# Kernel optimization log

Measured on AMD Instinct MI355X. Metric: run time of the kernel, lower is better.

The kernel has to match this reference:

```python
import jax, jax.numpy as jnp
import numpy as np
from jax import lax

N = 400000
INC = 128
MIDC = 64
OUTC = 128
KVOL = 27
EPS = 1e-5


def _bn(h, g, b, m, v):
    return (h - m) * (g * lax.rsqrt(v + EPS)) + b


def setup_inputs() -> dict:
    key = jax.random.key(0)
    ks = jax.random.split(key, 16)
    x = jax.random.normal(ks[0], (N, INC), jnp.float32)
    nb = jax.random.randint(ks[1], (KVOL, N), 0, N, jnp.int32)
    s1 = 1.0 / np.sqrt(INC)
    s2 = 1.0 / np.sqrt(MIDC * KVOL)
    s3 = 1.0 / np.sqrt(MIDC)
    w1 = jax.random.normal(ks[2], (INC, MIDC), jnp.float32) * s1
    w2 = jax.random.normal(ks[3], (KVOL, MIDC, MIDC), jnp.float32) * s2
    w3 = jax.random.normal(ks[4], (MIDC, OUTC), jnp.float32) * s3
    def bn_params(k, c):
        k1, k2, k3, k4 = jax.random.split(k, 4)
        return (jax.random.normal(k1, (c,), jnp.float32) * 0.1 + 1.0,
                jax.random.normal(k2, (c,), jnp.float32) * 0.1,
                jax.random.normal(k3, (c,), jnp.float32) * 0.1,
                jax.random.uniform(k4, (c,), jnp.float32) + 0.5)
    bn1_g, bn1_b, bn1_m, bn1_v = bn_params(ks[5], MIDC)
    bn2_g, bn2_b, bn2_m, bn2_v = bn_params(ks[6], MIDC)
    bn3_g, bn3_b, bn3_m, bn3_v = bn_params(ks[7], OUTC)
    return dict(x=x, nb=nb, w1=w1, w2=w2, w3=w3,
                bn1_g=bn1_g, bn1_b=bn1_b, bn1_m=bn1_m, bn1_v=bn1_v,
                bn2_g=bn2_g, bn2_b=bn2_b, bn2_m=bn2_m, bn2_v=bn2_v,
                bn3_g=bn3_g, bn3_b=bn3_b, bn3_m=bn3_m, bn3_v=bn3_v)


def reference(x, nb, w1, w2, w3,
              bn1_g, bn1_b, bn1_m, bn1_v,
              bn2_g, bn2_b, bn2_m, bn2_v,
              bn3_g, bn3_b, bn3_m, bn3_v):
    # 1x1 sparse conv == pointwise matmul
    h = jax.nn.relu(_bn(x @ w1, bn1_g, bn1_b, bn1_m, bn1_v))  # [N, midc]

    # ks=3 sparse conv: gather-matmul-accumulate over 27 kernel offsets
    def body(acc, kw):
        idx, wk = kw  # idx: [N] gather indices, wk: [midc, midc]
        return acc + h[idx] @ wk, None
    acc0 = jnp.zeros((N, MIDC), h.dtype)
    h2, _ = lax.scan(body, acc0, (nb, w2))
    h2 = jax.nn.relu(_bn(h2, bn2_g, bn2_b, bn2_m, bn2_v))

    # 1x1 conv + BN, then residual add (identity downsample: inc==outc, stride==1)
    h3 = _bn(h2 @ w3, bn3_g, bn3_b, bn3_m, bn3_v)  # [N, outc]
    return jax.nn.relu(h3 + x)
```

## Files before the change

kernel.cpp:

```cpp
#include <hip/hip_runtime.h>

#define N_PTS 400000
#define EPS 1e-5f
#define H_DELTA (11.0f / 255.0f)
#define H_INV_DELTA (255.0f / 11.0f)

typedef __attribute__((ext_vector_type(8))) short short8;
typedef __attribute__((ext_vector_type(4))) float f32x4;
typedef __attribute__((ext_vector_type(2))) float f32x2;
typedef __attribute__((ext_vector_type(2))) unsigned long long ull2;

constexpr size_t H_OFF   = 0;
constexpr size_t H2_OFF  = 51200000;
constexpr size_t W1T_OFF = 102400000;
constexpr size_t W2S_OFF = W1T_OFF + 16384;
constexpr size_t W3T_OFF = W2S_OFF + 221184;
constexpr size_t BNC_OFF = W3T_OFF + 16384;

__device__ __forceinline__ short f2bf(float f) {
  unsigned u = __builtin_bit_cast(unsigned, f);
  u += 0x7FFFu + ((u >> 16) & 1u);
  return (short)(u >> 16);
}

__device__ __forceinline__ unsigned cvtpk(float a, float b) {
  unsigned r;
  asm("v_cvt_pk_bf16_f32 %0, %1, %2" : "=v"(r) : "v"(a), "v"(b));
  return r;
}

__device__ __forceinline__ short8 q2bf(unsigned long long v) {
  unsigned lo = (unsigned)v, hi = (unsigned)(v >> 32);
  union { unsigned u[4]; short8 s8; } r;
  r.u[0] = cvtpk((float)(lo & 0xff), (float)((lo >> 8) & 0xff));
  r.u[1] = cvtpk((float)((lo >> 16) & 0xff), (float)(lo >> 24));
  r.u[2] = cvtpk((float)(hi & 0xff), (float)((hi >> 8) & 0xff));
  r.u[3] = cvtpk((float)((hi >> 16) & 0xff), (float)(hi >> 24));
  return r.s8;
}

__global__ __launch_bounds__(256) void prep_kernel(
    const float* __restrict__ w1, const float* __restrict__ w2,
    const float* __restrict__ w3,
    const float* __restrict__ g1, const float* __restrict__ b1,
    const float* __restrict__ m1, const float* __restrict__ v1,
    const float* __restrict__ g2, const float* __restrict__ b2,
    const float* __restrict__ m2, const float* __restrict__ v2,
    const float* __restrict__ g3, const float* __restrict__ b3,
    const float* __restrict__ m3, const float* __restrict__ v3,
    short* __restrict__ w1t, short* __restrict__ w2s,
    short* __restrict__ w3t, float* __restrict__ bnc) {
  int tid = blockIdx.x * 256 + threadIdx.x;
  int gs = gridDim.x * 256;
  for (int i = tid; i < 128 * 64; i += gs) {
    int k = i >> 6, n = i & 63;
    w1t[n * 128 + k] = f2bf(w1[i]);
  }
  for (int i = tid; i < 27 * 64 * 64; i += gs) {
    int kk = i >> 12, r = i & 4095, k = r >> 6, n = r & 63;
    int byte = (n * 64 + k) * 2;
    byte ^= (n & 7) << 4;
    w2s[kk * 4096 + (byte >> 1)] = f2bf(w2[i]);
  }
  for (int i = tid; i < 64 * 128; i += gs) {
    int k = i >> 7, n = i & 127;
    w3t[n * 64 + k] = f2bf(w3[i]);
  }
  if (tid < 64) {
    float s = g1[tid] * rsqrtf(v1[tid] + EPS);
    bnc[tid] = s; bnc[64 + tid] = b1[tid] - m1[tid] * s;
  } else if (tid < 128) {
    int c = tid - 64;
    float s = g2[c] * rsqrtf(v2[c] + EPS);
    bnc[128 + c] = s; bnc[192 + c] = b2[c] - m2[c] * s;
  } else if (tid < 256) {
    int c = tid - 128;
    float s = g3[c] * rsqrtf(v3[c] + EPS);
    bnc[256 + c] = s; bnc[384 + c] = b3[c] - m3[c] * s;
  }
}

__global__ __launch_bounds__(256) void stage1_kernel(
    const float* __restrict__ x, const short* __restrict__ w1t,
    const float* __restrict__ bnc, unsigned char* __restrict__ h) {
  __shared__ __align__(16) unsigned char t1[4][16][80];
  const int lane = threadIdx.x & 63;
  const int wid = threadIdx.x >> 6;
  const int lr = lane & 15, lk = lane >> 4;
  const long wbase = ((long)blockIdx.x * 4 + wid) * 64;
  if (wbase >= N_PTS) return;

  short8 bf[4][4];
#pragma unroll
  for (int nf = 0; nf < 4; ++nf)
#pragma unroll
    for (int ks = 0; ks < 4; ++ks)
      bf[nf][ks] = *(const short8*)(w1t + (nf * 16 + lr) * 128 + ks * 32 + lk * 8);

  float s[4], t[4];
#pragma unroll
  for (int nf = 0; nf < 4; ++nf) {
    int ch = nf * 16 + lr;
    s[nf] = bnc[ch]; t[nf] = bnc[64 + ch];
  }

#pragma unroll
  for (int mt = 0; mt < 4; ++mt) {
    f32x4 acc[4];
#pragma unroll
    for (int nf = 0; nf < 4; ++nf) acc[nf] = f32x4{0.f, 0.f, 0.f, 0.f};
    const float* xr = x + (wbase + mt * 16 + lr) * 128 + lk * 8;
#pragma unroll
    for (int ks = 0; ks < 4; ++ks) {
      f32x4 lo = *(const f32x4*)(xr + ks * 32);
      f32x4 hi = *(const f32x4*)(xr + ks * 32 + 4);
      union { unsigned u[4]; short8 s8; } av;
      av.u[0] = cvtpk(lo[0], lo[1]);
      av.u[1] = cvtpk(lo[2], lo[3]);
      av.u[2] = cvtpk(hi[0], hi[1]);
      av.u[3] = cvtpk(hi[2], hi[3]);
#pragma unroll
      for (int nf = 0; nf < 4; ++nf)
        acc[nf] = __builtin_amdgcn_mfma_f32_16x16x32_bf16(av.s8, bf[nf][ks], acc[nf], 0, 0, 0);
    }
#pragma unroll
    for (int nf = 0; nf < 4; ++nf) {
      int pos = (((nf & 1) * 2 + (lr >> 3)) << 4) + ((nf >> 1) << 3) + (lr & 7);
#pragma unroll
      for (int j = 0; j < 4; ++j) {
        float v = acc[nf][j] * s[nf] + t[nf];
        v = v > 0.f ? v : 0.f;
        unsigned qi = (unsigned)(v * H_INV_DELTA + 0.5f);
        if (qi > 255u) qi = 255u;
        t1[wid][lk * 4 + j][pos] = (unsigned char)qi;
      }
    }
    asm volatile("s_waitcnt lgkmcnt(0)" ::: "memory");
    __builtin_amdgcn_sched_barrier(0);
    {
      int row = lane >> 2, c = lane & 3;
      ull2 v = *(const ull2*)&t1[wid][row][c * 16];
      *(ull2*)(h + (wbase + mt * 16 + row) * 64 + c * 16) = v;
    }
    __builtin_amdgcn_sched_barrier(0);
  }
}

__global__ __launch_bounds__(256, 4) void stage2_kernel(
    const unsigned char* __restrict__ h, const int* __restrict__ nb,
    const short* __restrict__ w2s, const float* __restrict__ bnc,
    short* __restrict__ h2) {
  __shared__ __align__(16) short bbuf[2][4096];
  const int tid = threadIdx.x;
  const int lane = tid & 63;
  const int wid = tid >> 6;
  const int lr = lane & 15, lk = lane >> 4;
  const long wbase = ((long)blockIdx.x * 4 + wid) * 32;
  const int chunk = tid ^ ((tid >> 3) & 3);

  int boff[4][2];
#pragma unroll
  for (int nf = 0; nf < 4; ++nf) {
    int row = nf * 16 + lr;
#pragma unroll
    for (int ks = 0; ks < 2; ++ks)
      boff[nf][ks] = ((row * 128 + ks * 64 + lk * 16) ^ ((row & 7) << 4)) >> 1;
  }

  f32x4 acc[2][4];
#pragma unroll
  for (int mt = 0; mt < 2; ++mt)
#pragma unroll
    for (int nf = 0; nf < 4; ++nf) acc[mt][nf] = f32x4{0.f, 0.f, 0.f, 0.f};

  const int* nb0 = nb + wbase + lr;

  int idxq[4][2];
  ull2 acur[2], anext[2];

#pragma unroll
  for (int kk = 0; kk < 3; ++kk)
#pragma unroll
    for (int mt = 0; mt < 2; ++mt)
      idxq[kk][mt] = nb0[(long)kk * N_PTS + mt * 16];

#pragma unroll
  for (int mt = 0; mt < 2; ++mt)
    acur[mt] = *(const ull2*)(h + (long)idxq[0][mt] * 64 + lk * 16);

  {
    short8 b0a = *(const short8*)(w2s + chunk * 16);
    short8 b0b = *(const short8*)(w2s + chunk * 16 + 8);
    short8 b1a = *(const short8*)(w2s + 4096 + chunk * 16);
    short8 b1b = *(const short8*)(w2s + 4096 + chunk * 16 + 8);
    *(short8*)(&bbuf[0][chunk * 16]) = b0a;
    *(short8*)(&bbuf[0][chunk * 16 + 8]) = b0b;
    *(short8*)(&bbuf[1][chunk * 16]) = b1a;
    *(short8*)(&bbuf[1][chunk * 16 + 8]) = b1b;
  }
  asm volatile("s_waitcnt lgkmcnt(0)" ::: "memory");
  __builtin_amdgcn_s_barrier();

#pragma unroll
  for (int k = 0; k < 27; ++k) {
    const int kp = k & 1;
    short8 bsa, bsb;
    if (k + 2 < 27) {
      bsa = *(const short8*)(w2s + (k + 2) * 4096 + chunk * 16);
      bsb = *(const short8*)(w2s + (k + 2) * 4096 + chunk * 16 + 8);
    }
    if (k + 3 < 27) {
#pragma unroll
      for (int mt = 0; mt < 2; ++mt)
        idxq[(k + 3) & 3][mt] = nb0[(long)(k + 3) * N_PTS + mt * 16];
    }
    if (k + 1 < 27) {
#pragma unroll
      for (int mt = 0; mt < 2; ++mt)
        anext[mt] = *(const ull2*)(h + (long)idxq[(k + 1) & 3][mt] * 64 + lk * 16);
    }
    short8 af[2][2];
#pragma unroll
    for (int mt = 0; mt < 2; ++mt) {
      af[mt][0] = q2bf(acur[mt][0]);
      af[mt][1] = q2bf(acur[mt][1]);
    }
#pragma unroll
    for (int nf = 0; nf < 4; ++nf) {
#pragma unroll
      for (int ks = 0; ks < 2; ++ks) {
        short8 bfr = *(const short8*)(&bbuf[kp][boff[nf][ks]]);
#pragma unroll
        for (int mt = 0; mt < 2; ++mt)
          acc[mt][nf] = __builtin_amdgcn_mfma_f32_16x16x32_bf16(af[mt][ks], bfr, acc[mt][nf], 0, 0, 0);
      }
    }
    asm volatile("s_waitcnt lgkmcnt(0)" ::: "memory");
    __builtin_amdgcn_s_barrier();
    if (k + 2 < 27) {
      *(short8*)(&bbuf[kp][chunk * 16]) = bsa;
      *(short8*)(&bbuf[kp][chunk * 16 + 8]) = bsb;
    }
    if (k + 1 < 27) {
#pragma unroll
      for (int mt = 0; mt < 2; ++mt)
        acur[mt] = anext[mt];
    }
  }

  float s2[4], t2[4];
#pragma unroll
  for (int nf = 0; nf < 4; ++nf) {
    int ch = nf * 16 + lr;
    s2[nf] = bnc[128 + ch] * H_DELTA; t2[nf] = bnc[192 + ch];
  }

#pragma unroll
  for (int mt = 0; mt < 2; ++mt) {
    short* h2r = h2 + (wbase + mt * 16) * 64;
#pragma unroll
    for (int nf = 0; nf < 4; ++nf) {
      int ch = nf * 16 + lr;
#pragma unroll
      for (int j = 0; j < 4; ++j) {
        float v = acc[mt][nf][j] * s2[nf] + t2[nf];
        v = v > 0.f ? v : 0.f;
        h2r[(lk * 4 + j) * 64 + ch] = f2bf(v);
      }
    }
  }
}

__global__ __launch_bounds__(256) void stage3_kernel(
    const short* __restrict__ h2, const short* __restrict__ w3t,
    const float* __restrict__ bnc, const float* __restrict__ x,
    float* __restrict__ out) {
  __shared__ float tile3[4][16][130];
  const int lane = threadIdx.x & 63;
  const int wid = threadIdx.x >> 6;
  const int lr = lane & 15, lk = lane >> 4;
  const long wbase = ((long)blockIdx.x * 4 + wid) * 64;
  if (wbase >= N_PTS) return;

  short8 b3[8][2];
#pragma unroll
  for (int nf = 0; nf < 8; ++nf)
#pragma unroll
    for (int ks = 0; ks < 2; ++ks)
      b3[nf][ks] = *(const short8*)(w3t + (nf * 16 + lr) * 64 + ks * 32 + lk * 8);

  float s3[8], t3[8];
#pragma unroll
  for (int nf = 0; nf < 8; ++nf) {
    int ch = nf * 16 + lr;
    s3[nf] = bnc[256 + ch]; t3[nf] = bnc[384 + ch];
  }

#pragma unroll
  for (int mt = 0; mt < 4; ++mt) {
    short8 a3[2];
#pragma unroll
    for (int ks = 0; ks < 2; ++ks)
      a3[ks] = *(const short8*)(h2 + (wbase + mt * 16 + lr) * 64 + ks * 32 + lk * 8);

    f32x4 acc3[8];
#pragma unroll
    for (int nf = 0; nf < 8; ++nf) acc3[nf] = f32x4{0.f, 0.f, 0.f, 0.f};
#pragma unroll
    for (int ks = 0; ks < 2; ++ks)
#pragma unroll
      for (int nf = 0; nf < 8; ++nf)
        acc3[nf] = __builtin_amdgcn_mfma_f32_16x16x32_bf16(a3[ks], b3[nf][ks], acc3[nf], 0, 0, 0);

#pragma unroll
    for (int nf = 0; nf < 8; ++nf) {
      int ch = nf * 16 + lr;
#pragma unroll
      for (int j = 0; j < 4; ++j)
        tile3[wid][lk * 4 + j][ch] = acc3[nf][j] * s3[nf] + t3[nf];
    }
    asm volatile("s_waitcnt lgkmcnt(0)" ::: "memory");
    __builtin_amdgcn_sched_barrier(0);

    const float* xr = x + (wbase + mt * 16) * 128 + 2 * lane;
    float* outr = out + (wbase + mt * 16) * 128 + 2 * lane;
#pragma unroll
    for (int r = 0; r < 16; ++r) {
      f32x2 tv = *(const f32x2*)&tile3[wid][r][2 * lane];
      f32x2 xv = *(const f32x2*)(xr + r * 128);
      float v0 = tv[0] + xv[0]; v0 = v0 > 0.f ? v0 : 0.f;
      float v1 = tv[1] + xv[1]; v1 = v1 > 0.f ? v1 : 0.f;
      *(f32x2*)(outr + r * 128) = f32x2{v0, v1};
    }
    __builtin_amdgcn_sched_barrier(0);
  }
}

extern "C" void kernel_launch(void* const* d_in, const int* in_sizes, int n_in,
                              void* d_out, int out_size, void* d_ws, size_t ws_size,
                              hipStream_t stream) {
  const float* x  = (const float*)d_in[0];
  const int*   nb = (const int*)d_in[1];
  const float* w1 = (const float*)d_in[2];
  const float* w2 = (const float*)d_in[3];
  const float* w3 = (const float*)d_in[4];
  const float* g1 = (const float*)d_in[5];
  const float* b1 = (const float*)d_in[6];
  const float* m1 = (const float*)d_in[7];
  const float* v1 = (const float*)d_in[8];
  const float* g2 = (const float*)d_in[9];
  const float* b2 = (const float*)d_in[10];
  const float* m2 = (const float*)d_in[11];
  const float* v2 = (const float*)d_in[12];
  const float* g3 = (const float*)d_in[13];
  const float* b3 = (const float*)d_in[14];
  const float* m3 = (const float*)d_in[15];
  const float* v3 = (const float*)d_in[16];

  char* ws = (char*)d_ws;
  unsigned char* hbuf = (unsigned char*)(ws + H_OFF);
  short* h2buf = (short*)(ws + H2_OFF);
  short* w1t   = (short*)(ws + W1T_OFF);
  short* w2s   = (short*)(ws + W2S_OFF);
  short* w3t   = (short*)(ws + W3T_OFF);
  float* bnc   = (float*)(ws + BNC_OFF);
  float* outp  = (float*)d_out;

  prep_kernel<<<128, 256, 0, stream>>>(w1, w2, w3,
                                       g1, b1, m1, v1,
                                       g2, b2, m2, v2,
                                       g3, b3, m3, v3,
                                       w1t, w2s, w3t, bnc);
  stage1_kernel<<<1563, 256, 0, stream>>>(x, w1t, bnc, hbuf);
  stage2_kernel<<<3125, 256, 0, stream>>>(hbuf, nb, w2s, bnc, h2buf);
  stage3_kernel<<<1563, 256, 0, stream>>>(h2buf, w3t, bnc, x, outp);
}
```

Measured before the change: 328.4 us.

## Fuse stage3 pointwise conv and residual into stage2 epilogue

Stage 2's output tile is no longer written to a global bf16 buffer. It is staged per-wave in shared memory, reusing the gather B-buffer, and the 1x1 conv, BN3, residual add and ReLU run directly in the stage 2 epilogue. This drops one kernel launch and the write and re-read of the intermediate h2 tensor (about 51 MB each way). In exchange, stage 2 gets extra LDS (tile3) and more registers, which may lower occupancy under launch_bounds(256,4). W3 fragments are now reloaded from global or L2 per block instead of held in registers across four M-tiles.

```diff
diff --git a/kernel.cpp b/kernel.cpp
--- a/kernel.cpp
+++ b/kernel.cpp
@@ -11,7 +11,6 @@
 typedef __attribute__((ext_vector_type(2))) unsigned long long ull2;
 
 constexpr size_t H_OFF   = 0;
-constexpr size_t H2_OFF  = 51200000;
 constexpr size_t W1T_OFF = 102400000;
 constexpr size_t W2S_OFF = W1T_OFF + 16384;
 constexpr size_t W3T_OFF = W2S_OFF + 221184;
@@ -146,11 +145,13 @@
   }
 }
 
-__global__ __launch_bounds__(256, 4) void stage2_kernel(
+__global__ __launch_bounds__(256, 4) void stage23_kernel(
     const unsigned char* __restrict__ h, const int* __restrict__ nb,
-    const short* __restrict__ w2s, const float* __restrict__ bnc,
-    short* __restrict__ h2) {
+    const short* __restrict__ w2s, const short* __restrict__ w3t,
+    const float* __restrict__ bnc, const float* __restrict__ x,
+    float* __restrict__ out) {
   __shared__ __align__(16) short bbuf[2][4096];
+  __shared__ float tile3[4][16][130];
   const int tid = threadIdx.x;
   const int lane = tid & 63;
   const int wid = tid >> 6;
@@ -247,6 +248,7 @@
         acur[mt] = anext[mt];
     }
   }
+  short* tileA = ((short*)bbuf) + wid * (16 * 72);
 
   float s2[4], t2[4];
 #pragma unroll
@@ -257,7 +259,6 @@
 
 #pragma unroll
   for (int mt = 0; mt < 2; ++mt) {
-    short* h2r = h2 + (wbase + mt * 16) * 64;
 #pragma unroll
     for (int nf = 0; nf < 4; ++nf) {
       int ch = nf * 16 + lr;
@@ -265,59 +266,36 @@
       for (int j = 0; j < 4; ++j) {
         float v = acc[mt][nf][j] * s2[nf] + t2[nf];
         v = v > 0.f ? v : 0.f;
-        h2r[(lk * 4 + j) * 64 + ch] = f2bf(v);
+        tileA[(lk * 4 + j) * 72 + ch] = f2bf(v);
       }
     }
-  }
-}
-
-__global__ __launch_bounds__(256) void stage3_kernel(
-    const short* __restrict__ h2, const short* __restrict__ w3t,
-    const float* __restrict__ bnc, const float* __restrict__ x,
-    float* __restrict__ out) {
-  __shared__ float tile3[4][16][130];
-  const int lane = threadIdx.x & 63;
-  const int wid = threadIdx.x >> 6;
-  const int lr = lane & 15, lk = lane >> 4;
-  const long wbase = ((long)blockIdx.x * 4 + wid) * 64;
-  if (wbase >= N_PTS) return;
-
-  short8 b3[8][2];
-#pragma unroll
-  for (int nf = 0; nf < 8; ++nf)
+    asm volatile("s_waitcnt lgkmcnt(0)" ::: "memory");
+    __builtin_amdgcn_sched_barrier(0);
+
+    f32x4 acc3[8];
+#pragma unroll
+    for (int nf = 0; nf < 8; ++nf) acc3[nf] = f32x4{0.f, 0.f, 0.f, 0.f};
+    short8 a3[2];
 #pragma unroll
     for (int ks = 0; ks < 2; ++ks)
-      b3[nf][ks] = *(const short8*)(w3t + (nf * 16 + lr) * 64 + ks * 32 + lk * 8);
-
-  float s3[8], t3[8];
-#pragma unroll
-  for (int nf = 0; nf < 8; ++nf) {
-    int ch = nf * 16 + lr;
-    s3[nf] = bnc[256 + ch]; t3[nf] = bnc[384 + ch];
-  }
-
-#pragma unroll
-  for (int mt = 0; mt < 4; ++mt) {
-    short8 a3[2];
-#pragma unroll
-    for (int ks = 0; ks < 2; ++ks)
-      a3[ks] = *(const short8*)(h2 + (wbase + mt * 16 + lr) * 64 + ks * 32 + lk * 8);
-
-    f32x4 acc3[8];
-#pragma unroll
-    for (int nf = 0; nf < 8; ++nf) acc3[nf] = f32x4{0.f, 0.f, 0.f, 0.f};
-#pragma unroll
-    for (int ks = 0; ks < 2; ++ks)
-#pragma unroll
-      for (int nf = 0; nf < 8; ++nf)
-        acc3[nf] = __builtin_amdgcn_mfma_f32_16x16x32_bf16(a3[ks], b3[nf][ks], acc3[nf], 0, 0, 0);
+      a3[ks] = *(const short8*)&tileA[lr * 72 + ks * 32 + lk * 8];
+#pragma unroll
+    for (int nf = 0; nf < 8; ++nf) {
+#pragma unroll
+      for (int ks = 0; ks < 2; ++ks) {
+        short8 b3 = *(const short8*)(w3t + (nf * 16 + lr) * 64 + ks * 32 + lk * 8);
+        acc3[nf] = __builtin_amdgcn_mfma_f32_16x16x32_bf16(a3[ks], b3, acc3[nf], 0, 0, 0);
+      }
+    }
+    __builtin_amdgcn_sched_barrier(0);
 
 #pragma unroll
     for (int nf = 0; nf < 8; ++nf) {
       int ch = nf * 16 + lr;
+      float s3 = bnc[256 + ch], t3 = bnc[384 + ch];
 #pragma unroll
       for (int j = 0; j < 4; ++j)
-        tile3[wid][lk * 4 + j][ch] = acc3[nf][j] * s3[nf] + t3[nf];
+        tile3[wid][lk * 4 + j][ch] = acc3[nf][j] * s3 + t3;
     }
     asm volatile("s_waitcnt lgkmcnt(0)" ::: "memory");
     __builtin_amdgcn_sched_barrier(0);
@@ -359,7 +337,6 @@
 
   char* ws = (char*)d_ws;
   unsigned char* hbuf = (unsigned char*)(ws + H_OFF);
-  short* h2buf = (short*)(ws + H2_OFF);
   short* w1t   = (short*)(ws + W1T_OFF);
   short* w2s   = (short*)(ws + W2S_OFF);
   short* w3t   = (short*)(ws + W3T_OFF);
@@ -372,6 +349,5 @@
                                        g3, b3, m3, v3,
                                        w1t, w2s, w3t, bnc);
   stage1_kernel<<<1563, 256, 0, stream>>>(x, w1t, bnc, hbuf);
-  stage2_kernel<<<3125, 256, 0, stream>>>(hbuf, nb, w2s, bnc, h2buf);
-  stage3_kernel<<<1563, 256, 0, stream>>>(h2buf, w3t, bnc, x, outp);
-}
+  stage23_kernel<<<3125, 256, 0, stream>>>(hbuf, nb, w2s, w3t, bnc, x, outp);
+}
```

New measurement: 323.9 us. No clear change (-1.4%).
